# Optimization experiments

Hardware: AMD Instinct MI355X
Metric: run time of the kernel (lower is better)

The kernel has to match this reference:

```python
import jax, jax.numpy as jnp
import numpy as np

ANCHORS = np.array([[10.0, 13.0], [16.0, 30.0], [33.0, 23.0]], dtype=np.float32)
NUM_CLASSES = 80


def setup_inputs() -> dict:
    key = jax.random.key(0)
    B, g = 64, 52
    nA, nC = ANCHORS.shape[0], NUM_CLASSES
    x = jax.random.normal(key, (B, nA * (nC + 5), g, g), dtype=jnp.float32)
    return {"x": x, "img_dim": 416}


def reference(x, img_dim):
    anchors = jnp.asarray(ANCHORS)
    nA, nC = anchors.shape[0], NUM_CLASSES
    B = x.shape[0]
    g = x.shape[2]
    stride = img_dim / g

    # (B, nA, nC+5, g, g) -> (B, nA, g, g, nC+5)
    pred = x.reshape(B, nA, nC + 5, g, g).transpose(0, 1, 3, 4, 2)
    px = jax.nn.sigmoid(pred[..., 0])
    py = jax.nn.sigmoid(pred[..., 1])
    w = pred[..., 2]
    h = pred[..., 3]
    pred_conf = jax.nn.sigmoid(pred[..., 4])
    pred_cls = jax.nn.sigmoid(pred[..., 5:])

    grid = jnp.arange(g, dtype=x.dtype)
    grid_x = grid.reshape(1, 1, 1, g)  # broadcast over rows
    grid_y = grid.reshape(1, 1, g, 1)  # broadcast over cols
    scaled_anchors = anchors / stride
    anchor_w = scaled_anchors[:, 0].reshape(1, nA, 1, 1)
    anchor_h = scaled_anchors[:, 1].reshape(1, nA, 1, 1)

    # torch uses .data for box decode (detached)
    pred_boxes = jnp.stack(
        [
            jax.lax.stop_gradient(px) + grid_x,
            jax.lax.stop_gradient(py) + grid_y,
            jnp.exp(jax.lax.stop_gradient(w)) * anchor_w,
            jnp.exp(jax.lax.stop_gradient(h)) * anchor_h,
        ],
        axis=-1,
    )  # (B, nA, g, g, 4)

    output = jnp.concatenate(
        [
            pred_boxes.reshape(B, -1, 4) * stride,
            pred_conf.reshape(B, -1, 1),
            pred_cls.reshape(B, -1, nC),
        ],
        axis=-1,
    )
    return output
```

## Files before the change

kernel.cpp:

```cpp
#include <hip/hip_runtime.h>


#define G_     52
#define S_     (G_ * G_)
#define NA_    3
#define C_     85
#define B_     64
#define TS_    64
#define NTILES ((S_ + TS_ - 1) / TS_)

#define LOG2E_ 1.44269504088896340736f

__device__ __forceinline__ float fast_sigmoid(float v) {
    float e = __builtin_amdgcn_exp2f(-LOG2E_ * v);
    return __builtin_amdgcn_rcpf(1.0f + e);
}

__global__ __launch_bounds__(256) void yolo_decode_kernel(
    const float* __restrict__ x,
    const int*   __restrict__ img_dim_p,
    float*       __restrict__ out)
{
    __shared__ float lds[TS_ * C_];

    const int tile = blockIdx.x;
    const int a    = blockIdx.y;
    const int b    = blockIdx.z;
    const int s0   = tile * TS_;
    const int tid  = threadIdx.x;

    int   bits = img_dim_p[0];
    float img  = (bits > 0 && bits < (1 << 20)) ? (float)bits
                                                : __int_as_float(bits);
    const float stride = img / (float)G_;

    const float aw = (a == 0) ? 10.0f : (a == 1) ? 16.0f : 33.0f;
    const float ah = (a == 0) ? 13.0f : (a == 1) ? 30.0f : 23.0f;

    const float* inb = x + (size_t)(b * NA_ + a) * C_ * S_;
    const int ns = min(TS_, S_ - s0);
    const int nq = ns >> 2;

    for (int t = tid; t < C_ * (TS_ >> 2); t += 256) {
        const int c  = t >> 4;
        const int sq = t & 15;
        if (sq < nq) {
            float4 v = *reinterpret_cast<const float4*>(
                inb + (size_t)c * S_ + s0 + 4 * sq);
            float* vp = &v.x;

            if (c >= 4) {
                #pragma unroll
                for (int m = 0; m < 4; ++m) vp[m] = fast_sigmoid(vp[m]);
            } else if (c == 0) {
                #pragma unroll
                for (int m = 0; m < 4; ++m) {
                    const int sg = s0 + 4 * sq + m;
                    const int j  = sg % G_;
                    vp[m] = (fast_sigmoid(vp[m]) + (float)j) * stride;
                }
            } else if (c == 1) {
                #pragma unroll
                for (int m = 0; m < 4; ++m) {
                    const int sg = s0 + 4 * sq + m;
                    const int i  = sg / G_;
                    vp[m] = (fast_sigmoid(vp[m]) + (float)i) * stride;
                }
            } else if (c == 2) {
                #pragma unroll
                for (int m = 0; m < 4; ++m)
                    vp[m] = __builtin_amdgcn_exp2f(LOG2E_ * vp[m]) * aw;
            } else {
                #pragma unroll
                for (int m = 0; m < 4; ++m)
                    vp[m] = __builtin_amdgcn_exp2f(LOG2E_ * vp[m]) * ah;
            }

            const int sl = 4 * sq;
            lds[(sl    ) * C_ + c] = v.x;
            lds[(sl + 1) * C_ + c] = v.y;
            lds[(sl + 2) * C_ + c] = v.z;
            lds[(sl + 3) * C_ + c] = v.w;
        }
    }
    __syncthreads();

    const int nq4 = (ns * C_) >> 2;
    float* outb = out + ((size_t)(b * NA_ + a) * S_ + s0) * C_;

    for (int u = tid; u < nq4; u += 256) {
        const float4 v = *reinterpret_cast<const float4*>(&lds[4 * u]);
        *reinterpret_cast<float4*>(outb + 4 * u) = v;
    }
}

extern "C" void kernel_launch(void* const* d_in, const int* in_sizes, int n_in,
                              void* d_out, int out_size, void* d_ws, size_t ws_size,
                              hipStream_t stream)
{
    const float* x   = (const float*)d_in[0];
    const int*   img = (const int*)d_in[1];
    float*       out = (float*)d_out;

    dim3 grid(NTILES, NA_, B_);
    dim3 block(256);
    yolo_decode_kernel<<<grid, block, 0, stream>>>(x, img, out);
}
```

Measured before the change: 70.96 us.

## Process grid rows per block with register prefetch and double-buffered LDS

Each block now handles four full grid rows (52 cells × 85 channels) instead of a 64-cell tile. Every thread keeps five float4 loads in registers and prefetches the next row while the current one is transposed through a double-buffered LDS area. Output is written with nontemporal stores. The aim is to overlap global loads with the transpose and stores, and to drop the per-element div/mod work. In exchange there are fewer blocks, a barrier per row, and occupancy now depends on the larger register footprint.

```diff
diff --git a/kernel.cpp b/kernel.cpp
--- a/kernel.cpp
+++ b/kernel.cpp
@@ -1,15 +1,17 @@
 #include <hip/hip_runtime.h>
 
 
-#define G_     52
-#define S_     (G_ * G_)
-#define NA_    3
-#define C_     85
-#define B_     64
-#define TS_    64
-#define NTILES ((S_ + TS_ - 1) / TS_)
+#define G_        52
+#define S_        2704
+#define NA_       3
+#define C_        85
+#define B_        64
+#define ROW_WORDS (G_ * C_)
+#define ITEMS     (ROW_WORDS / 4)
+#define ROWS_PB   4
+#define LOG2E_    1.44269504088896340736f
 
-#define LOG2E_ 1.44269504088896340736f
+typedef float f32x4 __attribute__((ext_vector_type(4)));
 
 __device__ __forceinline__ float fast_sigmoid(float v) {
     float e = __builtin_amdgcn_exp2f(-LOG2E_ * v);
@@ -21,13 +23,13 @@
     const int*   __restrict__ img_dim_p,
     float*       __restrict__ out)
 {
-    __shared__ float lds[TS_ * C_];
+    __shared__ float lds[2][ROW_WORDS];
 
-    const int tile = blockIdx.x;
-    const int a    = blockIdx.y;
-    const int b    = blockIdx.z;
-    const int s0   = tile * TS_;
-    const int tid  = threadIdx.x;
+    const int rb  = blockIdx.x;
+    const int a   = blockIdx.y;
+    const int b   = blockIdx.z;
+    const int tid = threadIdx.x;
+    const int row0 = rb * ROWS_PB;
 
     int   bits = img_dim_p[0];
     float img  = (bits > 0 && bits < (1 << 20)) ? (float)bits
@@ -37,60 +39,85 @@
     const float aw = (a == 0) ? 10.0f : (a == 1) ? 16.0f : 33.0f;
     const float ah = (a == 0) ? 13.0f : (a == 1) ? 30.0f : 23.0f;
 
-    const float* inb = x + (size_t)(b * NA_ + a) * C_ * S_;
-    const int ns = min(TS_, S_ - s0);
-    const int nq = ns >> 2;
+    const float* inb   = x   + (size_t)(b * NA_ + a) * (size_t)(C_ * S_);
+    float*       outb0 = out + (size_t)(b * NA_ + a) * (size_t)S_ * C_;
 
-    for (int t = tid; t < C_ * (TS_ >> 2); t += 256) {
-        const int c  = t >> 4;
-        const int sq = t & 15;
-        if (sq < nq) {
-            float4 v = *reinterpret_cast<const float4*>(
-                inb + (size_t)c * S_ + s0 + 4 * sq);
-            float* vp = &v.x;
+    int c_[5], sq_[5];
+    #pragma unroll
+    for (int i = 0; i < 5; ++i) {
+        const int q = tid + 256 * i;
+        c_[i]  = q / 13;
+        sq_[i] = q - 13 * c_[i];
+    }
+    const bool act4 = (tid < ITEMS - 1024);
 
-            if (c >= 4) {
-                #pragma unroll
-                for (int m = 0; m < 4; ++m) vp[m] = fast_sigmoid(vp[m]);
-            } else if (c == 0) {
-                #pragma unroll
-                for (int m = 0; m < 4; ++m) {
-                    const int sg = s0 + 4 * sq + m;
-                    const int j  = sg % G_;
-                    vp[m] = (fast_sigmoid(vp[m]) + (float)j) * stride;
+    f32x4 regs[5];
+
+    #pragma unroll
+    for (int i = 0; i < 5; ++i)
+        if (i < 4 || act4)
+            regs[i] = *reinterpret_cast<const f32x4*>(
+                inb + (size_t)c_[i] * S_ + row0 * G_ + 4 * sq_[i]);
+
+    for (int r = 0; r < ROWS_PB; ++r) {
+        const int row  = row0 + r;
+        float*    buf  = lds[r & 1];
+        const float rowf = (float)row;
+
+        #pragma unroll
+        for (int i = 0; i < 5; ++i) {
+            if (i < 4 || act4) {
+                const int c  = c_[i];
+                const int sq = sq_[i];
+                f32x4 v = regs[i];
+                if (c >= 4) {
+                    #pragma unroll
+                    for (int m = 0; m < 4; ++m) v[m] = fast_sigmoid(v[m]);
+                } else if (c == 0) {
+                    #pragma unroll
+                    for (int m = 0; m < 4; ++m)
+                        v[m] = (fast_sigmoid(v[m]) + (float)(4 * sq + m)) * stride;
+                } else if (c == 1) {
+                    #pragma unroll
+                    for (int m = 0; m < 4; ++m)
+                        v[m] = (fast_sigmoid(v[m]) + rowf) * stride;
+                } else if (c == 2) {
+                    #pragma unroll
+                    for (int m = 0; m < 4; ++m)
+                        v[m] = __builtin_amdgcn_exp2f(LOG2E_ * v[m]) * aw;
+                } else {
+                    #pragma unroll
+                    for (int m = 0; m < 4; ++m)
+                        v[m] = __builtin_amdgcn_exp2f(LOG2E_ * v[m]) * ah;
                 }
-            } else if (c == 1) {
-                #pragma unroll
-                for (int m = 0; m < 4; ++m) {
-                    const int sg = s0 + 4 * sq + m;
-                    const int i  = sg / G_;
-                    vp[m] = (fast_sigmoid(vp[m]) + (float)i) * stride;
-                }
-            } else if (c == 2) {
-                #pragma unroll
-                for (int m = 0; m < 4; ++m)
-                    vp[m] = __builtin_amdgcn_exp2f(LOG2E_ * vp[m]) * aw;
-            } else {
-                #pragma unroll
-                for (int m = 0; m < 4; ++m)
-                    vp[m] = __builtin_amdgcn_exp2f(LOG2E_ * vp[m]) * ah;
+                const int base = 4 * sq * C_ + c;
+                buf[base         ] = v[0];
+                buf[base +     C_] = v[1];
+                buf[base + 2 * C_] = v[2];
+                buf[base + 3 * C_] = v[3];
             }
+        }
 
-            const int sl = 4 * sq;
-            lds[(sl    ) * C_ + c] = v.x;
-            lds[(sl + 1) * C_ + c] = v.y;
-            lds[(sl + 2) * C_ + c] = v.z;
-            lds[(sl + 3) * C_ + c] = v.w;
+        if (r + 1 < ROWS_PB) {
+            #pragma unroll
+            for (int i = 0; i < 5; ++i)
+                if (i < 4 || act4)
+                    regs[i] = *reinterpret_cast<const f32x4*>(
+                        inb + (size_t)c_[i] * S_ + (row + 1) * G_ + 4 * sq_[i]);
         }
-    }
-    __syncthreads();
 
-    const int nq4 = (ns * C_) >> 2;
-    float* outb = out + ((size_t)(b * NA_ + a) * S_ + s0) * C_;
+        asm volatile("s_waitcnt lgkmcnt(0)" ::: "memory");
+        __builtin_amdgcn_s_barrier();
 
-    for (int u = tid; u < nq4; u += 256) {
-        const float4 v = *reinterpret_cast<const float4*>(&lds[4 * u]);
-        *reinterpret_cast<float4*>(outb + 4 * u) = v;
+        float* outr = outb0 + (size_t)row * ROW_WORDS;
+        #pragma unroll
+        for (int i = 0; i < 5; ++i) {
+            if (i < 4 || act4) {
+                const int q = tid + 256 * i;
+                const f32x4 v = *reinterpret_cast<const f32x4*>(&buf[4 * q]);
+                __builtin_nontemporal_store(v, reinterpret_cast<f32x4*>(outr + 4 * q));
+            }
+        }
     }
 }
 
@@ -102,7 +129,7 @@
     const int*   img = (const int*)d_in[1];
     float*       out = (float*)d_out;
 
-    dim3 grid(NTILES, NA_, B_);
+    dim3 grid(G_ / ROWS_PB / 1, NA_, B_);
     dim3 block(256);
-    yolo_decode_kernel<<<grid, block, 0, stream>>>(x, img, out);
+    yolo_decode_kernel<<<dim3(13, NA_, B_), block, 0, stream>>>(x, img, out);
 }
```

Result: faster. 63.35 us (-10.7%).
